# Kernel tuning notes

Hardware: AMD Instinct MI355X
Metric: run time of the kernel (lower is better)

Reference implementation:

```python
import jax, jax.numpy as jnp
import numpy as np
from jax.scipy.special import xlogy

LAMBDA_XM = 0.05
LAMBDA_SEG2D = 1.0
BN_EPS = 1e-5


def setup_inputs() -> dict:
    key = jax.random.key(0)
    ks = jax.random.split(key, 40)
    S, N, Nv, B, Np, M, H, C, MID = 2, 240000, 80000, 2, 120000, 30000, 64, 20, 16
    Nimg = B * M
    f = lambda i, shape, s=0.05: jax.random.normal(ks[i], shape, jnp.float32) * s
    inp = {
        'img_feat': f(0, (S, Nimg, H), 1.0),
        'pts_feat': f(1, (S, Nv, H), 1.0),
        'coors_inv': jax.random.randint(ks[2], (S, N), 0, Nv),
        'labels': jax.random.randint(ks[3], (N,), 0, C),
        'img_label': jax.random.randint(ks[4], (Nimg,), 0, C),
        'p2img_idx': jax.random.randint(ks[5], (B, M), 0, Np),
        # multihead 3d classifiers (per scale): Linear(H,128)-ReLU-Linear(128,C)
        'w3a': f(6, (S, H, 128)), 'b3a': jnp.zeros((S, 128)),
        'w3b': f(7, (S, 128, C)), 'b3b': jnp.zeros((S, C)),
        # multihead fuse classifiers
        'wfa': f(8, (S, H, 128)), 'bfa': jnp.zeros((S, 128)),
        'wfb': f(9, (S, 128, C)), 'bfb': jnp.zeros((S, C)),
        # attention: fc1(H->H//4), fc2(H->H//4), fc3(H//2->2), conv1/conv2 (1x1 -> linear) + BN
        'fc1w': f(10, (S, H, MID)), 'fc1b': jnp.zeros((S, MID)),
        'fc2w': f(11, (S, H, MID)), 'fc2b': jnp.zeros((S, MID)),
        'fc3w': f(12, (S, 2 * MID, 2)), 'fc3b': jnp.zeros((S, 2)),
        'c1w': f(13, (S, H, H)), 'c1b': jnp.zeros((S, H)),
        'bn1g': jnp.ones((S, H)), 'bn1b': jnp.zeros((S, H)),
        'c2w': f(14, (S, H, H)), 'c2b': jnp.zeros((S, H)),
        'bn2g': jnp.ones((S, H)), 'bn2b': jnp.zeros((S, H)),
        # final classifier Linear(S*H,128)-ReLU-Linear(128,C)
        'clw1': f(15, (S * H, 128)), 'clb1': jnp.zeros((128,)),
        'clw2': f(16, (128, C)), 'clb2': jnp.zeros((C,)),
    }
    return inp


def _mlp2(x, w1, b1, w2, b2):
    return jax.nn.relu(x @ w1 + b1) @ w2 + b2


def _ce(logits, lab):
    logp = jax.nn.log_softmax(logits, -1)
    return -jnp.take_along_axis(logp, lab[:, None], axis=1).mean()


def _lovasz(probs, lab):
    # lovasz-softmax over all classes, averaged over present classes
    C = probs.shape[1]
    fg = jax.nn.one_hot(lab, C, dtype=probs.dtype)  # [N,C]
    errors = jnp.abs(fg - probs)

    def per_class(err_c, fg_c):
        order = jnp.argsort(-err_c)
        e = err_c[order]
        f = fg_c[order]
        gts = f.sum()
        inter = gts - jnp.cumsum(f)
        union = gts + jnp.cumsum(1.0 - f)
        jac = 1.0 - inter / union
        jac = jnp.concatenate([jac[:1], jac[1:] - jac[:-1]])
        return jnp.dot(e, jac)

    losses = jax.vmap(per_class)(errors.T, fg.T)  # [C]
    present = (fg.sum(0) > 0).astype(probs.dtype)
    return jnp.sum(losses * present) / jnp.maximum(present.sum(), 1.0)


def _seg_loss(logits, lab):
    return _ce(logits, lab) + _lovasz(jax.nn.softmax(logits, -1), lab)


def _convbn_relu(x, cw, cb, g, b):
    # 1x1 Conv1d == per-point linear; BN (training-mode batch stats over points)
    y = x @ cw + cb
    mu = y.mean(0)
    var = y.var(0)
    return jax.nn.relu((y - mu) * jax.lax.rsqrt(var + BN_EPS) * g + b)


def reference(img_feat, pts_feat, coors_inv, labels, img_label, p2img_idx,
              w3a, b3a, w3b, b3b, wfa, bfa, wfb, bfb,
              fc1w, fc1b, fc2w, fc2b, fc3w, fc3b,
              c1w, c1b, bn1g, bn1b, c2w, c2b, bn2g, bn2b,
              clw1, clb1, clw2, clb2):
    S, Nv, H = pts_feat.shape
    C = w3b.shape[-1]
    B, M = p2img_idx.shape
    N = labels.shape[0]
    Np = N // B
    # p2img_mapping: per-batch gather composed to one global gather (batch blocks are contiguous/equal)
    gidx = (jnp.arange(B)[:, None] * Np + p2img_idx).reshape(-1)  # [Nimg]

    loss = jnp.float32(0.0)
    feats = []
    for s in range(S):
        pred3d = _mlp2(pts_feat[s], w3a[s], b3a[s], w3b[s], b3b[s])  # [Nv,C]
        # voxelize_labels: majority vote per voxel (== unique+scatter_max count argmax)
        counts = jnp.zeros((Nv, C), jnp.float32).at[coors_inv[s], labels].add(1.0)
        vox_lab = jnp.argmax(counts, axis=1)  # [Nv]
        # gather voxel feats/preds to image-projected points (fused gather)
        idx = coors_inv[s][gidx]  # [Nimg]
        p = pts_feat[s][idx]      # [Nimg,H] pseudo feats
        pts_pred = pred3d[idx]    # [Nimg,C]
        v = img_feat[s]           # [Nimg,H] valid (image) feats
        # Attention fusion
        w = jax.nn.sigmoid(
            jnp.concatenate([p @ fc1w[s] + fc1b[s], v @ fc2w[s] + fc2b[s]], -1) @ fc3w[s] + fc3b[s])  # [Nimg,2]
        fuse = (_convbn_relu(p, c1w[s], c1b[s], bn1g[s], bn1b[s]) * w[:, 0:1]
                + _convbn_relu(v, c2w[s], c2b[s], bn2g[s], bn2b[s]) * w[:, 1:2])
        feats.append(fuse)
        fuse_pred = _mlp2(fuse, wfa[s], bfa[s], wfb[s], bfb[s])
        loss = loss + _seg_loss(pred3d, vox_lab)
        loss = loss + _seg_loss(fuse_pred, img_label) * LAMBDA_SEG2D / S
        # F.kl_div(log_softmax(pts_pred), softmax(fuse_pred)), reduction='mean' over all elements
        pf = jax.nn.softmax(fuse_pred, -1)
        kl = jnp.mean(xlogy(pf, pf) - pf * jax.nn.log_softmax(pts_pred, -1))
        loss = loss + kl * LAMBDA_XM / S
    img_logits = _mlp2(jnp.concatenate(feats, -1), clw1, clb1, clw2, clb2)
    loss = loss + _seg_loss(img_logits, img_label)
    return loss
```

## Files before the change

kernel.cpp:

```cpp
#include <hip/hip_runtime.h>
#include <stdint.h>

static constexpr int NV   = 80000;
static constexpr int NPT  = 240000;
static constexpr int NIMG = 60000;
static constexpr int Hh   = 64;
static constexpr int Cc   = 20;
static constexpr int NPp  = 120000;
static constexpr int Mm   = 30000;
static constexpr int NB     = 8192;
static constexpr int NCH    = 16;
static constexpr int NBLK_GA  = (NIMG + 63) / 64;
static constexpr int NBLK_MLP = NV / 64;
static constexpr int NBLK_CNT = (NPT + 255) / 256;
static constexpr int NBLK_FILL_NV = (NV + 255) / 256;
static constexpr int NBLK_FILL_NI = (NIMG + 255) / 256;
static constexpr int NBLK_HIST = Cc * NCH;
static constexpr int NBLK_IDX  = (NIMG + 255) / 256;
#define BN_EPS 1e-5f

using bf16x8 = __attribute__((ext_vector_type(8))) short;
using f32x4  = __attribute__((ext_vector_type(4))) float;

__device__ __forceinline__ float waveReduce(float v) {
  #pragma unroll
  for (int o = 32; o > 0; o >>= 1) v += __shfl_down(v, o);
  return v;
}
__device__ __forceinline__ short f2bf(float f) {
  uint32_t u = __float_as_uint(f);
  return (short)((u + 0x7FFFu + ((u >> 16) & 1u)) >> 16);
}
__device__ __forceinline__ float bf2f(uint32_t h) { return __uint_as_float(h << 16); }
__device__ __forceinline__ uint32_t pk2(float a, float b) {
  return ((uint32_t)(uint16_t)f2bf(a)) | ((uint32_t)(uint16_t)f2bf(b) << 16);
}

struct PackDesc { const float* src; short* dst; int K, Nr, nt; };
struct PackArgs { PackDesc d[14]; };

__global__ void __launch_bounds__(256)
k_pack_zero(PackArgs pa,
            const float* __restrict__ fc1w, const float* __restrict__ fc1b,
            const float* __restrict__ fc2w, const float* __restrict__ fc2b,
            const float* __restrict__ fc3w, const float* __restrict__ fc3b,
            float* __restrict__ attEffs,
            uint4* __restrict__ zb, int zq,
            const int* __restrict__ ci0, const int* __restrict__ ci1,
            const int* __restrict__ p2img,
            int* __restrict__ idx0, int* __restrict__ idx1) {
  int bid = blockIdx.x;
  if (bid >= 384) {
    bid -= 384;
    if (bid < NBLK_IDX) {
      int i = bid * 256 + threadIdx.x;
      if (i < NIMG) idx0[i] = ci0[(i >= Mm ? NPp : 0) + p2img[i]];
    } else {
      int i = (bid - NBLK_IDX) * 256 + threadIdx.x;
      if (i < NIMG) idx1[i] = ci1[(i >= Mm ? NPp : 0) + p2img[i]];
    }
    return;
  }
  if (bid >= 128) {
    const uint4 z = make_uint4(0u, 0u, 0u, 0u);
    int i = (bid - 128) * 256 + threadIdx.x;
    for (; i < zq; i += 256 * 256) zb[i] = z;
    return;
  }
  const int stride = 128 * 256;
  for (int di = 0; di < 14; di++) {
    const float* src = pa.d[di].src;
    short* dst = pa.d[di].dst;
    int K = pa.d[di].K, Nr = pa.d[di].Nr, ntiles = pa.d[di].nt;
    int total = (K / 32) * ntiles * 512;
    for (int idx = bid * 256 + threadIdx.x; idx < total; idx += stride) {
      int j = idx & 7, lane = (idx >> 3) & 63, tile = idx >> 9;
      int nt = tile % ntiles, kt = tile / ntiles;
      int k = kt * 32 + (lane >> 4) * 8 + j;
      int n = nt * 16 + (lane & 15);
      float v = (n < Nr) ? src[(size_t)k * Nr + n] : 0.f;
      dst[idx] = f2bf(v);
    }
  }
  if (bid < 2 && threadIdx.x < 64) {
    int s = bid, t = threadIdx.x;
    const float* f1w = fc1w + s * 64 * 16; const float* f1b = fc1b + s * 16;
    const float* f2w = fc2w + s * 64 * 16; const float* f2b = fc2b + s * 16;
    const float* f3w = fc3w + s * 64;      const float* f3b = fc3b + s * 2;
    float* aE = attEffs + s * 320;
    float p0 = 0.f, p1 = 0.f, v0 = 0.f, v1 = 0.f;
    #pragma unroll
    for (int j = 0; j < 16; j++) {
      p0 = fmaf(f1w[t * 16 + j], f3w[j * 2], p0);
      p1 = fmaf(f1w[t * 16 + j], f3w[j * 2 + 1], p1);
      v0 = fmaf(f2w[t * 16 + j], f3w[(16 + j) * 2], v0);
      v1 = fmaf(f2w[t * 16 + j], f3w[(16 + j) * 2 + 1], v1);
    }
    aE[t * 2] = p0; aE[t * 2 + 1] = p1;
    aE[128 + t * 2] = v0; aE[128 + t * 2 + 1] = v1;
    if (t == 0) {
      float b0 = f3b[0], b1 = f3b[1];
      for (int j = 0; j < 16; j++) {
        b0 += f1b[j] * f3w[j * 2] + f2b[j] * f3w[(16 + j) * 2];
        b1 += f1b[j] * f3w[j * 2 + 1] + f2b[j] * f3w[(16 + j) * 2 + 1];
      }
      aE[256] = b0; aE[257] = b1;
    }
  }
}

__device__ void scanbin_body(const uint32_t* __restrict__ Hb, const uint32_t* __restrict__ HFb,
                             int n, int call, float* __restrict__ lossesC5,
                             int* __restrict__ gts5, int cls) {
  __shared__ int sWC[4], sWF[4];
  __shared__ float sRedF[4];
  int t = threadIdx.x;
  int lane = t & 63, w = t >> 6;
  const uint32_t* Hc  = Hb  + (size_t)cls * NB;
  const uint32_t* HFc = HFb + (size_t)cls * NB;
  int locC = 0, locF = 0;
  #pragma unroll
  for (int i = 0; i < 8; i++) {
    uint4 cv = *(const uint4*)(Hc  + t * 32 + i * 4);
    uint4 fv = *(const uint4*)(HFc + t * 32 + i * 4);
    locC += (int)(cv.x + cv.y + cv.z + cv.w);
    locF += (int)(fv.x + fv.y + fv.z + fv.w);
  }
  int sc = locC, sf = locF;
  #pragma unroll
  for (int o = 1; o < 64; o <<= 1) {
    int a = __shfl_up(sc, o);
    int b = __shfl_up(sf, o);
    if (lane >= o) { sc += a; sf += b; }
  }
  if (lane == 63) { sWC[w] = sc; sWF[w] = sf; }
  __syncthreads();
  int offC = 0, offF = 0, Ftot = 0;
  #pragma unroll
  for (int ww = 0; ww < 4; ww++) {
    int fc = sWF[ww];
    Ftot += fc;
    if (ww < w) { offC += sWC[ww]; offF += fc; }
  }
  int runC = offC + sc - locC;
  int runF = offF + sf - locF;
  float gts = (float)Ftot;
  float contrib = 0.f;
  #pragma unroll
  for (int i = 0; i < 8; i++) {
    uint4 cv = *(const uint4*)(Hc  + t * 32 + i * 4);
    uint4 fv = *(const uint4*)(HFc + t * 32 + i * 4);
    uint32_t ca[4] = {cv.x, cv.y, cv.z, cv.w};
    uint32_t fa[4] = {fv.x, fv.y, fv.z, fv.w};
    #pragma unroll
    for (int j = 0; j < 4; j++) {
      int cnt = (int)ca[j], fgc = (int)fa[j];
      runC += cnt; runF += fgc;
      if (cnt > 0 && Ftot > 0) {
        float r0 = (float)(n - runC);
        float F0 = (float)(Ftot - runF);
        float r1 = r0 + (float)cnt;
        float F1 = F0 + (float)fgc;
        float emean = __uint_as_float((uint32_t)(t * 32 + i * 4 + j) << 17);
        contrib += emean * (r1 / (gts + r1 - F1) - r0 / (gts + r0 - F0));
      }
    }
  }
  contrib = waveReduce(contrib);
  if (lane == 0) sRedF[w] = contrib;
  __syncthreads();
  if (t == 0) {
    lossesC5[call * 32 + cls] = (Ftot > 0) ? (sRedF[0] + sRedF[1] + sRedF[2] + sRedF[3]) : 0.f;
    gts5[call * 32 + cls] = Ftot;
  }
}

template<int D>
__device__ __forceinline__ void mfma_mlp_body(const short* sXb, short* sH,
    int r0, int rows,
    const short* __restrict__ pw1, const float* __restrict__ B1,
    const short* __restrict__ pw2, const float* __restrict__ B2,
    float* __restrict__ Out) {
  constexpr int LDB = D + 8;
  constexpr int KT1 = D / 32;
  const int t = threadIdx.x;
  const int lane = t & 63, w = t >> 6;
  const int m = lane & 15, quad = lane >> 4;
  const int rowA = 16 * w + m;
  bf16x8 a1[KT1];
  #pragma unroll
  for (int kt = 0; kt < KT1; kt++)
    a1[kt] = *(const bf16x8*)(sXb + rowA * LDB + kt * 32 + quad * 8);
  const bf16x8* b1 = (const bf16x8*)pw1;
  #pragma unroll
  for (int nt = 0; nt < 8; nt++) {
    f32x4 c = {0.f, 0.f, 0.f, 0.f};
    #pragma unroll
    for (int kt = 0; kt < KT1; kt++)
      c = __builtin_amdgcn_mfma_f32_16x16x32_bf16(a1[kt], b1[(kt * 8 + nt) * 64 + lane], c, 0, 0, 0);
    int col = nt * 16 + m;
    float bc = B1[col];
    #pragma unroll
    for (int reg = 0; reg < 4; reg++)
      sH[(16 * w + quad * 4 + reg) * 136 + col] = f2bf(fmaxf(c[reg] + bc, 0.f));
  }
  __syncthreads();
  bf16x8 a2[4];
  #pragma unroll
  for (int kt = 0; kt < 4; kt++)
    a2[kt] = *(const bf16x8*)(sH + rowA * 136 + kt * 32 + quad * 8);
  const bf16x8* b2 = (const bf16x8*)pw2;
  #pragma unroll
  for (int nt = 0; nt < 2; nt++) {
    f32x4 c = {0.f, 0.f, 0.f, 0.f};
    #pragma unroll
    for (int kt = 0; kt < 4; kt++)
      c = __builtin_amdgcn_mfma_f32_16x16x32_bf16(a2[kt], b2[(kt * 2 + nt) * 64 + lane], c, 0, 0, 0);
    int col = nt * 16 + m;
    if (col < Cc) {
      float bc = B2[col];
      #pragma unroll
      for (int reg = 0; reg < 4; reg++) {
        int gr = r0 + 16 * w + quad * 4 + reg;
        if (gr < rows) Out[(size_t)gr * Cc + col] = c[reg] + bc;
      }
    }
  }
}

__device__ void mlp64_body(int bid0, const float* __restrict__ X,
    const short* __restrict__ pw1, const float* __restrict__ B1,
    const short* __restrict__ pw2, const float* __restrict__ B2,
    float* __restrict__ Out, int rows, char* smem) {
  short* sXb = (short*)smem;
  short* sH  = (short*)(smem + 9216);
  int t = threadIdx.x, r0 = bid0 * 64;
  for (int i = t; i < 1024; i += 256) {
    int r = i >> 4, k4 = (i & 15) * 4;
    int gr = r0 + r;
    float4 v = (gr < rows) ? *(const float4*)(X + (size_t)gr * 64 + k4)
                           : make_float4(0.f, 0.f, 0.f, 0.f);
    uint2 p; p.x = pk2(v.x, v.y); p.y = pk2(v.z, v.w);
    *(uint2*)(sXb + r * 72 + k4) = p;
  }
  __syncthreads();
  mfma_mlp_body<64>(sXb, sH, r0, rows, pw1, B1, pw2, B2, Out);
}

__device__ void mlp128_body(int bid0, const uint16_t* __restrict__ Xh,
    const short* __restrict__ pw1, const float* __restrict__ B1,
    const short* __restrict__ pw2, const float* __restrict__ B2,
    float* __restrict__ Out, char* smem) {
  short* sXb = (short*)smem;
  short* sH  = (short*)(smem + 17408);
  int t = threadIdx.x, r0 = bid0 * 64;
  for (int i = t; i < 2048; i += 256) {
    int r = i >> 5, k4 = (i & 31) * 4;
    int gr = r0 + r;
    uint2 p = (gr < NIMG) ? *(const uint2*)(Xh + (size_t)gr * 128 + k4) : make_uint2(0u, 0u);
    *(uint2*)(sXb + r * 136 + k4) = p;
  }
  __syncthreads();
  mfma_mlp_body<128>(sXb, sH, r0, NIMG, pw1, B1, pw2, B2, Out);
}

__device__ void cnt_body(int bid0, const int* __restrict__ ci, const int* __restrict__ labels,
                         int* __restrict__ counts) {
  int i = bid0 * 256 + threadIdx.x;
  if (i < NPT) atomicAdd(&counts[(size_t)ci[i] * Cc + labels[i]], 1);
}

__device__ void colred_body(int bid0, const float* __restrict__ partials,
                            float* __restrict__ red64) {
  int t = threadIdx.x, j = bid0;
  float v = 0.f;
  for (int b = j; b < NBLK_GA; b += 64) v += partials[(size_t)b * 256 + t];
  red64[j * 256 + t] = v;
}

__device__ void fill_body(int bid0, const float* __restrict__ logits,
                          const int* __restrict__ lab, const int* __restrict__ vcnt,
                          int n, uint16_t* __restrict__ E,
                          float ceScale, float* __restrict__ lossAcc,
                          const float* __restrict__ pred3d, const int* __restrict__ idxg,
                          float klScale) {
  int i = bid0 * 256 + threadIdx.x;
  float total = 0.f;
  if (i < n) {
    int lb;
    if (vcnt) {
      const int* crow = vcnt + (size_t)i * Cc;
      int best = crow[0], arg = 0;
      #pragma unroll
      for (int k = 1; k < Cc; k++) {
        int ck = crow[k];
        if (ck > best) { best = ck; arg = k; }
      }
      lb = arg;
    } else {
      lb = lab[i];
    }
    const float* l = logits + (size_t)i * Cc;
    float m = l[0];
    #pragma unroll
    for (int c = 1; c < Cc; c++) m = fmaxf(m, l[c]);
    float ex[Cc]; float se = 0.f;
    #pragma unroll
    for (int c = 0; c < Cc; c++) { ex[c] = expf(l[c] - m); se += ex[c]; }
    float inv = 1.f / se;
    float lse = logf(se);
    total = -(l[lb] - m - lse) * ceScale;
    #pragma unroll
    for (int c = 0; c < Cc; c++) {
      float prob = ex[c] * inv;
      int fg = (c == lb) ? 1 : 0;
      float err = fg ? (1.f - prob) : prob;
      err = fmaxf(err, 0.f);
      uint32_t key = __float_as_uint(err) >> 17;
      E[(size_t)c * n + i] = (uint16_t)((key << 1) | (uint32_t)fg);
    }
    if (pred3d) {
      const float* q = pred3d + (size_t)idxg[i] * Cc;
      float mq = q[0];
      #pragma unroll
      for (int c = 1; c < Cc; c++) mq = fmaxf(mq, q[c]);
      float sq = 0.f;
      #pragma unroll
      for (int c = 0; c < Cc; c++) sq += expf(q[c] - mq);
      float lsq = logf(sq);
      float kl = 0.f;
      #pragma unroll
      for (int c = 0; c < Cc; c++) {
        float lf = l[c] - m - lse;
        float pf = ex[c] * inv;
        float lq = q[c] - mq - lsq;
        kl += pf * (lf - lq);
      }
      total += kl * klScale;
    }
  }
  total = waveReduce(total);
  __shared__ float sh[4];
  int lane = threadIdx.x & 63, w = threadIdx.x >> 6;
  if (lane == 0) sh[w] = total;
  __syncthreads();
  if (threadIdx.x == 0) atomicAdd(lossAcc, sh[0] + sh[1] + sh[2] + sh[3]);
}

__device__ void hist_body(int bid0, const uint16_t* __restrict__ E, int n,
                          uint32_t* __restrict__ H, uint32_t* __restrict__ HF, char* smem) {
  uint32_t* lcf = (uint32_t*)smem;
  int t = threadIdx.x;
  int cls = bid0 / NCH, ch = bid0 - cls * NCH;
  int CHsz = (n + NCH - 1) / NCH;
  int i0 = ch * CHsz;
  int i1 = min(n, i0 + CHsz);
  for (int b = t; b < NB; b += 256) lcf[b] = 0u;
  __syncthreads();
  const uint16_t* Ec = E + (size_t)cls * n;
  for (int i = i0 + t; i < i1; i += 256) {
    uint32_t p = Ec[i];
    atomicAdd(&lcf[p >> 1], 0x10000u | (p & 1u));
  }
  __syncthreads();
  uint32_t* Hc  = H  + (size_t)cls * NB;
  uint32_t* HFc = HF + (size_t)cls * NB;
  for (int b = t; b < NB; b += 256) {
    uint32_t v = lcf[b];
    if (v) {
      atomicAdd(&Hc[b], v >> 16);
      uint32_t f = v & 0xFFFFu;
      if (f) atomicAdd(&HFc[b], f);
    }
  }
}

__device__ void gatt_body(int bid0, const float* __restrict__ pts, const int* __restrict__ idx,
                          const float* __restrict__ img,
                          const short* __restrict__ pc1, const float* __restrict__ c1b,
                          const short* __restrict__ pc2, const float* __restrict__ c2b,
                          const float* __restrict__ attEff,
                          uint16_t* __restrict__ y1, uint16_t* __restrict__ y2,
                          float* __restrict__ attw, float* __restrict__ partials,
                          char* smem) {
  short* sP = (short*)smem;
  short* sV = (short*)(smem + 9216);
  float* sAtt  = (float*)(smem + 18432);
  float* sStat = (float*)(smem + 20480);
  int t = threadIdx.x;
  int r0 = bid0 * 64;
  for (int i = t; i < 1024; i += 256) {
    int r = i >> 4, q = i & 15;
    int gr = r0 + r;
    float4 vp = make_float4(0.f, 0.f, 0.f, 0.f), vv = vp;
    if (gr < NIMG) {
      vp = *(const float4*)(pts + (size_t)idx[gr] * 64 + q * 4);
      vv = *(const float4*)(img + (size_t)gr * 64 + q * 4);
    }
    uint2 pp, qv;
    pp.x = pk2(vp.x, vp.y); pp.y = pk2(vp.z, vp.w);
    qv.x = pk2(vv.x, vv.y); qv.y = pk2(vv.z, vv.w);
    *(uint2*)(sP + r * 72 + q * 4) = pp;
    *(uint2*)(sV + r * 72 + q * 4) = qv;
  }
  __syncthreads();
  {
    int r = t & 63, qq = t >> 6;
    const float* aP = attEff;
    const float* aV = attEff + 128;
    float l0 = 0.f, l1 = 0.f;
    for (int k = qq * 16; k < qq * 16 + 16; k += 4) {
      uint2 up = *(const uint2*)(sP + r * 72 + k);
      uint2 uv = *(const uint2*)(sV + r * 72 + k);
      float p0 = bf2f(up.x & 0xffff), p1 = bf2f(up.x >> 16);
      float p2 = bf2f(up.y & 0xffff), p3 = bf2f(up.y >> 16);
      float v0 = bf2f(uv.x & 0xffff), v1 = bf2f(uv.x >> 16);
      float v2 = bf2f(uv.y & 0xffff), v3 = bf2f(uv.y >> 16);
      float4 wa = *(const float4*)(aP + 2 * k);
      float4 wb = *(const float4*)(aP + 2 * k + 4);
      l0 += p0 * wa.x + p1 * wa.z + p2 * wb.x + p3 * wb.z;
      l1 += p0 * wa.y + p1 * wa.w + p2 * wb.y + p3 * wb.w;
      float4 ua = *(const float4*)(aV + 2 * k);
      float4 ub = *(const float4*)(aV + 2 * k + 4);
      l0 += v0 * ua.x + v1 * ua.z + v2 * ub.x + v3 * ub.z;
      l1 += v0 * ua.y + v1 * ua.w + v2 * ub.y + v3 * ub.w;
    }
    sAtt[r * 8 + qq * 2] = l0;
    sAtt[r * 8 + qq * 2 + 1] = l1;
  }
  const int lane = t & 63, w = t >> 6;
  const int m = lane & 15, quad = lane >> 4;
  const int rowA = 16 * w + m;
  bf16x8 ap[2], av[2];
  #pragma unroll
  for (int kt = 0; kt < 2; kt++) {
    ap[kt] = *(const bf16x8*)(sP + rowA * 72 + kt * 32 + quad * 8);
    av[kt] = *(const bf16x8*)(sV + rowA * 72 + kt * 32 + quad * 8);
  }
  const bf16x8* b1 = (const bf16x8*)pc1;
  const bf16x8* b2 = (const bf16x8*)pc2;
  #pragma unroll
  for (int nt = 0; nt < 4; nt++) {
    int col = nt * 16 + m;
    f32x4 c1 = {0.f, 0.f, 0.f, 0.f}, c2 = {0.f, 0.f, 0.f, 0.f};
    #pragma unroll
    for (int kt = 0; kt < 2; kt++) {
      c1 = __builtin_amdgcn_mfma_f32_16x16x32_bf16(ap[kt], b1[(kt * 4 + nt) * 64 + lane], c1, 0, 0, 0);
      c2 = __builtin_amdgcn_mfma_f32_16x16x32_bf16(av[kt], b2[(kt * 4 + nt) * 64 + lane], c2, 0, 0, 0);
    }
    float bb1 = c1b[col], bb2 = c2b[col];
    float s1 = 0.f, q1 = 0.f, s2 = 0.f, q2 = 0.f;
    #pragma unroll
    for (int reg = 0; reg < 4; reg++) {
      int gr = r0 + 16 * w + quad * 4 + reg;
      if (gr < NIMG) {
// ... 48 lines not shown
    float* __restrict__ Out, char* smem) {
  short* sXb = (short*)smem;
  short* sH  = (short*)(smem + 9216);
  float* sBn = (float*)(smem + 9216 + 17408);
  int t = threadIdx.x, r0 = bid0 * 64;
  float acc = 0.f;
  #pragma unroll 8
  for (int b = 0; b < 64; b++) acc += red64[b * 256 + t];
  float* sSum = (float*)sH;
  sSum[t] = acc;
  __syncthreads();
  if (t < 64) {
    float nn = (float)NIMG;
    float mu1 = sSum[t] / nn;
    float var1 = sSum[64 + t] / nn - mu1 * mu1;
    float a1 = g1[t] / sqrtf(var1 + BN_EPS);
    sBn[t] = a1; sBn[64 + t] = be1[t] - mu1 * a1;
    float mu2 = sSum[128 + t] / nn;
    float var2 = sSum[192 + t] / nn - mu2 * mu2;
    float a2 = g2[t] / sqrtf(var2 + BN_EPS);
    sBn[128 + t] = a2; sBn[192 + t] = be2[t] - mu2 * a2;
  }
  __syncthreads();
  for (int i = t; i < 1024; i += 256) {
    int r = i >> 4, q = i & 15;
    int gr = r0 + r;
    uint2 zp = make_uint2(0u, 0u);
    if (gr < NIMG) {
      float4 a1 = *(const float4*)(sBn + q * 4);
      float4 c1 = *(const float4*)(sBn + 64 + q * 4);
      float4 a2 = *(const float4*)(sBn + 128 + q * 4);
      float4 c2 = *(const float4*)(sBn + 192 + q * 4);
      uint2 u1 = *(const uint2*)(y1 + (size_t)gr * 64 + q * 4);
      uint2 u2 = *(const uint2*)(y2 + (size_t)gr * 64 + q * 4);
      float w0 = attw[gr * 2], w1 = attw[gr * 2 + 1];
      float zx = fmaxf(fmaf(bf2f(u1.x & 0xffff), a1.x, c1.x), 0.f) * w0
               + fmaxf(fmaf(bf2f(u2.x & 0xffff), a2.x, c2.x), 0.f) * w1;
      float zy = fmaxf(fmaf(bf2f(u1.x >> 16),   a1.y, c1.y), 0.f) * w0
               + fmaxf(fmaf(bf2f(u2.x >> 16),   a2.y, c2.y), 0.f) * w1;
      float zz = fmaxf(fmaf(bf2f(u1.y & 0xffff), a1.z, c1.z), 0.f) * w0
               + fmaxf(fmaf(bf2f(u2.y & 0xffff), a2.z, c2.z), 0.f) * w1;
      float zw = fmaxf(fmaf(bf2f(u1.y >> 16),   a1.w, c1.w), 0.f) * w0
               + fmaxf(fmaf(bf2f(u2.y >> 16),   a2.w, c2.w), 0.f) * w1;
      zp.x = pk2(zx, zy); zp.y = pk2(zz, zw);
      *(uint2*)(feats + (size_t)gr * 128 + s64 + q * 4) = zp;
    }
    *(uint2*)(sXb + r * 72 + q * 4) = zp;
  }
  __syncthreads();
  mfma_mlp_body<64>(sXb, sH, r0, NIMG, pw1, B1, pw2, B2, Out);
}

__global__ void __launch_bounds__(256)
k_mega2(const float* __restrict__ pf0, const float* __restrict__ pf1,
        const int* __restrict__ idx0, const int* __restrict__ idx1,
        const float* __restrict__ if0, const float* __restrict__ if1,
        const short* pc1w0, const short* pc1w1, const short* pc2w0, const short* pc2w1,
        const float* c1b, const float* c2b, const float* attEffs,
        uint16_t* y1a, uint16_t* y2a, uint16_t* y1b, uint16_t* y2b,
        float* attw0, float* attw1, float* partials0, float* partials1,
        const short* pw3a0, const float* b3a, const short* pw3b0, const float* b3b,
        const short* pw3a1, const short* pw3b1,
        float* pred3d0, float* pred3d1,
        const int* __restrict__ ci0, const int* __restrict__ ci1,
        const int* __restrict__ labels,
        int* __restrict__ counts0, int* __restrict__ counts1) {
  __shared__ char smem[26624];
  int bid = blockIdx.x;
  if (bid < NBLK_GA) {
    gatt_body(bid, pf0, idx0, if0, pc1w0, c1b, pc2w0, c2b, attEffs,
              y1a, y2a, attw0, partials0, smem);
    return;
  }
  bid -= NBLK_GA;
  if (bid < NBLK_GA) {
    gatt_body(bid, pf1, idx1, if1, pc1w1, c1b + 64, pc2w1, c2b + 64, attEffs + 320,
              y1b, y2b, attw1, partials1, smem);
    return;
  }
  bid -= NBLK_GA;
  if (bid < NBLK_MLP) { mlp64_body(bid, pf0, pw3a0, b3a, pw3b0, b3b, pred3d0, NV, smem); return; }
  bid -= NBLK_MLP;
  if (bid < NBLK_MLP) { mlp64_body(bid, pf1, pw3a1, b3a + 128, pw3b1, b3b + Cc, pred3d1, NV, smem); return; }
  bid -= NBLK_MLP;
  if (bid < NBLK_CNT) { cnt_body(bid, ci0, labels, counts0); return; }
  cnt_body(bid - NBLK_CNT, ci1, labels, counts1);
}

__global__ void __launch_bounds__(256)
k_fill_colred(const float* __restrict__ l0, const int* __restrict__ vc0, uint16_t* __restrict__ E0,
              const float* __restrict__ l1, const int* __restrict__ vc1, uint16_t* __restrict__ E1,
              float ce, float* __restrict__ lossAcc,
              const float* partials0, float* red64_0,
              const float* partials1, float* red64_1) {
  int bid = blockIdx.x;
  if (bid < NBLK_FILL_NV) {
    fill_body(bid, l0, nullptr, vc0, NV, E0, ce, lossAcc, nullptr, nullptr, 0.f);
    return;
  }
  bid -= NBLK_FILL_NV;
  if (bid < NBLK_FILL_NV) {
    fill_body(bid, l1, nullptr, vc1, NV, E1, ce, lossAcc, nullptr, nullptr, 0.f);
    return;
  }
  bid -= NBLK_FILL_NV;
  if (bid < 64) { colred_body(bid, partials0, red64_0); return; }
  colred_body(bid - 64, partials1, red64_1);
}

__global__ void __launch_bounds__(256)
k_fuse2_hist2(const uint16_t* y1a, const uint16_t* y2a, const float* attw0, const float* red64_0,
              const uint16_t* y1b, const uint16_t* y2b, const float* attw1, const float* red64_1,
              const float* bn1g, const float* bn1b, const float* bn2g, const float* bn2b,
              uint16_t* feats,
              const short* pwfa0, const float* bfa, const short* pwfb0, const float* bfb,
              const short* pwfa1, const short* pwfb1,
              float* fusepred0, float* fusepred1,
              const uint16_t* __restrict__ E0, uint32_t* H0, uint32_t* HF0,
              const uint16_t* __restrict__ E1, uint32_t* H2, uint32_t* HF2) {
  __shared__ char smem[32768];
  int bid = blockIdx.x;
  if (bid < NBLK_GA) {
    fusemlp_body(bid, y1a, y2a, attw0, red64_0, bn1g, bn1b, bn2g, bn2b, feats, 0,
                 pwfa0, bfa, pwfb0, bfb, fusepred0, smem);
    return;
  }
  bid -= NBLK_GA;
  if (bid < NBLK_GA) {
    fusemlp_body(bid, y1b, y2b, attw1, red64_1, bn1g + 64, bn1b + 64, bn2g + 64, bn2b + 64,
                 feats, 64, pwfa1, bfa + 128, pwfb1, bfb + Cc, fusepred1, smem);
    return;
  }
  bid -= NBLK_GA;
  if (bid < NBLK_HIST) { hist_body(bid, E0, NV, H0, HF0, smem); return; }
  hist_body(bid - NBLK_HIST, E1, NV, H2, HF2, smem);
}

__global__ void __launch_bounds__(256)
k_finx2(const uint16_t* __restrict__ feats,
        const short* pcl1, const float* clb1, const short* pcl2, const float* clb2,
        float* finalpred,
        const float* fusepred0, const float* pred3d0, const int* idx0, uint16_t* E0w,
        const float* fusepred1, const float* pred3d1, const int* idx1, uint16_t* E1w,
        const int* __restrict__ img_label, float ce, float kl, float* lossAcc,
        const uint32_t* H0, const uint32_t* HF0,
        const uint32_t* H2, const uint32_t* HF2,
        float* lossesC5, int* gts5) {
  __shared__ char smem[34816];
  int bid = blockIdx.x;
  if (bid < NBLK_GA) { mlp128_body(bid, feats, pcl1, clb1, pcl2, clb2, finalpred, smem); return; }
  bid -= NBLK_GA;
  if (bid < NBLK_FILL_NI) {
    fill_body(bid, fusepred0, img_label, nullptr, NIMG, E0w, ce, lossAcc, pred3d0, idx0, kl);
    return;
  }
  bid -= NBLK_FILL_NI;
  if (bid < NBLK_FILL_NI) {
    fill_body(bid, fusepred1, img_label, nullptr, NIMG, E1w, ce, lossAcc, pred3d1, idx1, kl);
    return;
  }
  bid -= NBLK_FILL_NI;
  if (bid < Cc) { scanbin_body(H0, HF0, NV, 0, lossesC5, gts5, bid); return; }
  scanbin_body(H2, HF2, NV, 2, lossesC5, gts5, bid - Cc);
}

__global__ void __launch_bounds__(256)
k_hist2_fill(const uint16_t* __restrict__ E0, uint32_t* H1, uint32_t* HF1,
             const uint16_t* __restrict__ E1, uint32_t* H3, uint32_t* HF3,
             const float* __restrict__ finalpred, const int* __restrict__ img_label,
             uint16_t* __restrict__ E2, float ce, float* lossAcc) {
  __shared__ char smem[32768];
  int bid = blockIdx.x;
  if (bid < NBLK_HIST) { hist_body(bid, E0, NIMG, H1, HF1, smem); return; }
  bid -= NBLK_HIST;
  if (bid < NBLK_HIST) { hist_body(bid, E1, NIMG, H3, HF3, smem); return; }
  fill_body(bid - NBLK_HIST, finalpred, img_label, nullptr, NIMG, E2, ce, lossAcc,
            nullptr, nullptr, 0.f);
}

__global__ void __launch_bounds__(256)
k_hist_scan2(const uint16_t* __restrict__ E2, uint32_t* H4, uint32_t* HF4,
             const uint32_t* H1, const uint32_t* HF1,
             const uint32_t* H3, const uint32_t* HF3,
             float* lossesC5, int* gts5) {
  __shared__ char smem[32768];
  int bid = blockIdx.x;
  if (bid < NBLK_HIST) { hist_body(bid, E2, NIMG, H4, HF4, smem); return; }
  bid -= NBLK_HIST;
  if (bid < Cc) { scanbin_body(H1, HF1, NIMG, 1, lossesC5, gts5, bid); return; }
  scanbin_body(H3, HF3, NIMG, 3, lossesC5, gts5, bid - Cc);
}

__global__ void __launch_bounds__(256)
k_scanbin5(const uint32_t* Hb, const uint32_t* HFb, int n, int call,
           float* lossesC5, int* gts5) {
  scanbin_body(Hb, HFb, n, call, lossesC5, gts5, blockIdx.x);
}

__global__ void k_final(const float* __restrict__ lossAcc,
                        const float* __restrict__ lossesC5, const int* __restrict__ gts5,
                        float* __restrict__ out) {
  const float coefs[5] = {1.0f, 0.5f, 1.0f, 0.5f, 1.0f};
  float loss = lossAcc[0];
  for (int call = 0; call < 5; call++) {
    float s = 0.f; int np = 0;
    for (int c = 0; c < Cc; c++)
      if (gts5[call * 32 + c] > 0) { s += lossesC5[call * 32 + c]; np++; }
    loss += coefs[call] * s / (float)(np > 0 ? np : 1);
  }
  out[0] = loss;
}

extern "C" void kernel_launch(void* const* d_in, const int* in_sizes, int n_in,
                              void* d_out, int out_size, void* d_ws, size_t ws_size,
                              hipStream_t stream) {
  const float* img_feat = (const float*)d_in[0];
  const float* pts_feat = (const float*)d_in[1];
  const int* coors_inv  = (const int*)d_in[2];
  const int* labels     = (const int*)d_in[3];
  const int* img_label  = (const int*)d_in[4];
  const int* p2img      = (const int*)d_in[5];
  const float* w3a = (const float*)d_in[6];
  const float* b3a = (const float*)d_in[7];
  const float* w3b = (const float*)d_in[8];
  const float* b3b = (const float*)d_in[9];
  const float* wfa = (const float*)d_in[10];
  const float* bfa = (const float*)d_in[11];
  const float* wfb = (const float*)d_in[12];
  const float* bfb = (const float*)d_in[13];
  const float* fc1w = (const float*)d_in[14];
  const float* fc1b = (const float*)d_in[15];
  const float* fc2w = (const float*)d_in[16];
  const float* fc2b = (const float*)d_in[17];
  const float* fc3w = (const float*)d_in[18];
  const float* fc3b = (const float*)d_in[19];
  const float* c1w  = (const float*)d_in[20];
  const float* c1b  = (const float*)d_in[21];
  const float* bn1g = (const float*)d_in[22];
  const float* bn1b = (const float*)d_in[23];
  const float* c2w  = (const float*)d_in[24];
  const float* c2b  = (const float*)d_in[25];
  const float* bn2g = (const float*)d_in[26];
  const float* bn2b = (const float*)d_in[27];
  const float* clw1 = (const float*)d_in[28];
  const float* clb1 = (const float*)d_in[29];
  const float* clw2 = (const float*)d_in[30];
  const float* clb2 = (const float*)d_in[31];
  (void)in_sizes; (void)n_in; (void)out_size; (void)ws_size;

  char* ws = (char*)d_ws;
  size_t off = 0;
  auto alloc = [&](size_t bytes) { void* p = ws + off; off += (bytes + 255) & ~(size_t)255; return p; };
  uint16_t* feats = (uint16_t*)alloc((size_t)NIMG * 128 * 2);
  float* pred3d0 = (float*)alloc((size_t)NV * Cc * 4);
  float* pred3d1 = (float*)alloc((size_t)NV * Cc * 4);
  int* idx0 = (int*)alloc((size_t)NIMG * 4);
  int* idx1 = (int*)alloc((size_t)NIMG * 4);
  uint16_t* y1a = (uint16_t*)alloc((size_t)NIMG * Hh * 2);
  uint16_t* y2a = (uint16_t*)alloc((size_t)NIMG * Hh * 2);
  uint16_t* y1b = (uint16_t*)alloc((size_t)NIMG * Hh * 2);
  uint16_t* y2b = (uint16_t*)alloc((size_t)NIMG * Hh * 2);
  uint16_t* E0 = (uint16_t*)alloc((size_t)Cc * NV * 2);
  uint16_t* E1 = (uint16_t*)alloc((size_t)Cc * NV * 2);
  uint16_t* E2 = (uint16_t*)alloc((size_t)Cc * NIMG * 2);
  float* partials0 = (float*)alloc((size_t)NBLK_GA * 256 * 4);
  float* partials1 = (float*)alloc((size_t)NBLK_GA * 256 * 4);
  float* red64_0 = (float*)alloc(64 * 256 * 4);
  float* red64_1 = (float*)alloc(64 * 256 * 4);
  float* attw0 = (float*)alloc((size_t)NIMG * 2 * 4);
  float* attw1 = (float*)alloc((size_t)NIMG * 2 * 4);
  float* fusepred0 = (float*)alloc((size_t)NIMG * Cc * 4);
  float* fusepred1 = (float*)alloc((size_t)NIMG * Cc * 4);
  float* finalpred = (float*)alloc((size_t)NIMG * Cc * 4);
  short* pwAll = (short*)alloc(86016 * 2);
  short* pw3a0 = pwAll,          * pw3a1 = pwAll + 8192;
  short* pwfa0 = pwAll + 16384,  * pwfa1 = pwAll + 24576;
  short* pw3b0 = pwAll + 32768,  * pw3b1 = pwAll + 36864;
  short* pwfb0 = pwAll + 40960,  * pwfb1 = pwAll + 45056;
  short* pcl1  = pwAll + 49152;
  short* pcl2  = pwAll + 65536;
  short* pc1w0 = pwAll + 69632,  * pc1w1 = pwAll + 73728;
  short* pc2w0 = pwAll + 77824,  * pc2w1 = pwAll + 81920;
  float* attEffs = (float*)alloc(2 * 320 * 4);
  size_t zsize = 1024 + (size_t)5 * 2 * Cc * NB * 4 + (size_t)2 * NV * Cc * 4;
  char* zbase = (char*)alloc(zsize);
  float* lossAcc  = (float*)zbase;
  float* lossesC5 = (float*)zbase + 32;
  int*   gts5     = (int*)((float*)zbase + 192);
  uint32_t* Hbase = (uint32_t*)(zbase + 1024);
  auto Hc  = [&](int call) { return Hbase + (size_t)call * 2 * Cc * NB; };
  auto HFc = [&](int call) { return Hbase + (size_t)call * 2 * Cc * NB + (size_t)Cc * NB; };
  int* counts0 = (int*)(zbase + 1024 + (size_t)5 * 2 * Cc * NB * 4);
  int* counts1 = counts0 + (size_t)NV * Cc;
  int zq = (int)(zsize / 16);

  const float kl = 0.025f / ((float)NIMG * Cc);
  const float* pf0 = pts_feat;
  const float* pf1 = pts_feat + (size_t)NV * Hh;
  const float* if0 = img_feat;
  const float* if1 = img_feat + (size_t)NIMG * Hh;
  const int* ci0 = coors_inv;
  const int* ci1 = coors_inv + NPT;

  PackArgs pa;
  pa.d[0]  = {w3a,        pw3a0, 64, 128, 8};
  pa.d[1]  = {w3a + 8192, pw3a1, 64, 128, 8};
  pa.d[2]  = {wfa,        pwfa0, 64, 128, 8};
  pa.d[3]  = {wfa + 8192, pwfa1, 64, 128, 8};
  pa.d[4]  = {w3b,        pw3b0, 128, 20, 2};
  pa.d[5]  = {w3b + 2560, pw3b1, 128, 20, 2};
  pa.d[6]  = {wfb,        pwfb0, 128, 20, 2};
  pa.d[7]  = {wfb + 2560, pwfb1, 128, 20, 2};
  pa.d[8]  = {clw1,       pcl1, 128, 128, 8};
  pa.d[9]  = {clw2,       pcl2, 128, 20, 2};
  pa.d[10] = {c1w,        pc1w0, 64, 64, 4};
  pa.d[11] = {c1w + 4096, pc1w1, 64, 64, 4};
  pa.d[12] = {c2w,        pc2w0, 64, 64, 4};
  pa.d[13] = {c2w + 4096, pc2w1, 64, 64, 4};
  k_pack_zero<<<384 + 2 * NBLK_IDX, 256, 0, stream>>>(
      pa, fc1w, fc1b, fc2w, fc2b, fc3w, fc3b, attEffs,
      (uint4*)zbase, zq, ci0, ci1, p2img, idx0, idx1);

  k_mega2<<<2 * NBLK_GA + 2 * NBLK_MLP + 2 * NBLK_CNT, 256, 0, stream>>>(
      pf0, pf1, idx0, idx1, if0, if1,
      pc1w0, pc1w1, pc2w0, pc2w1, c1b, c2b, attEffs,
      y1a, y2a, y1b, y2b, attw0, attw1, partials0, partials1,
      pw3a0, b3a, pw3b0, b3b, pw3a1, pw3b1, pred3d0, pred3d1,
      ci0, ci1, labels, counts0, counts1);

  k_fill_colred<<<2 * NBLK_FILL_NV + 128, 256, 0, stream>>>(
      pred3d0, counts0, E0, pred3d1, counts1, E1, 1.0f / NV, lossAcc,
      partials0, red64_0, partials1, red64_1);

  k_fuse2_hist2<<<2 * NBLK_GA + 2 * NBLK_HIST, 256, 0, stream>>>(
      y1a, y2a, attw0, red64_0, y1b, y2b, attw1, red64_1,
      bn1g, bn1b, bn2g, bn2b, feats,
      pwfa0, bfa, pwfb0, bfb, pwfa1, pwfb1, fusepred0, fusepred1,
      E0, Hc(0), HFc(0), E1, Hc(2), HFc(2));

  k_finx2<<<NBLK_GA + 2 * NBLK_FILL_NI + 2 * Cc, 256, 0, stream>>>(
      feats, pcl1, clb1, pcl2, clb2, finalpred,
      fusepred0, pred3d0, idx0, E0,
      fusepred1, pred3d1, idx1, E1,
      img_label, 0.5f / NIMG, kl, lossAcc,
      Hc(0), HFc(0), Hc(2), HFc(2), lossesC5, gts5);

  k_hist2_fill<<<2 * NBLK_HIST + NBLK_FILL_NI, 256, 0, stream>>>(
      E0, Hc(1), HFc(1), E1, Hc(3), HFc(3),
      finalpred, img_label, E2, 1.0f / NIMG, lossAcc);

  k_hist_scan2<<<NBLK_HIST + 2 * Cc, 256, 0, stream>>>(
      E2, Hc(4), HFc(4), Hc(1), HFc(1), Hc(3), HFc(3), lossesC5, gts5);

  k_scanbin5<<<Cc, 256, 0, stream>>>(Hc(4), HFc(4), NIMG, 4, lossesC5, gts5);

  k_final<<<1, 1, 0, stream>>>(lossAcc, lossesC5, gts5, (float*)d_out);
}
```

Baseline: 347.1 us.

## Pre-convert point features to bf16, pack histograms into 64-bit bins, interleave blocks

```diff
diff --git a/kernel.cpp b/kernel.cpp
--- a/kernel.cpp
+++ b/kernel.cpp
@@ -17,6 +17,7 @@
 static constexpr int NBLK_FILL_NI = (NIMG + 255) / 256;
 static constexpr int NBLK_HIST = Cc * NCH;
 static constexpr int NBLK_IDX  = (NIMG + 255) / 256;
+static constexpr int NBLK_CVT  = 1280;
 #define BN_EPS 1e-5f
 
 using bf16x8 = __attribute__((ext_vector_type(8))) short;
@@ -48,8 +49,24 @@
             uint4* __restrict__ zb, int zq,
             const int* __restrict__ ci0, const int* __restrict__ ci1,
             const int* __restrict__ p2img,
-            int* __restrict__ idx0, int* __restrict__ idx1) {
+            int* __restrict__ idx0, int* __restrict__ idx1,
+            const float* __restrict__ pts, uint16_t* __restrict__ ptsbf) {
   int bid = blockIdx.x;
+  if (bid >= 384 + 2 * NBLK_IDX) {
+    int i = (bid - 384 - 2 * NBLK_IDX) * 256 + threadIdx.x;
+    const int total8 = 2 * NV * 64 / 8;
+    const int strideC = NBLK_CVT * 256;
+    for (; i < total8; i += strideC) {
+      const float* s = pts + (size_t)i * 8;
+      float4 a = *(const float4*)s;
+      float4 b = *(const float4*)(s + 4);
+      uint4 o;
+      o.x = pk2(a.x, a.y); o.y = pk2(a.z, a.w);
+      o.z = pk2(b.x, b.y); o.w = pk2(b.z, b.w);
+      *(uint4*)(ptsbf + (size_t)i * 8) = o;
+    }
+    return;
+  }
   if (bid >= 384) {
     bid -= 384;
     if (bid < NBLK_IDX) {
@@ -109,22 +126,20 @@
   }
 }
 
-__device__ void scanbin_body(const uint32_t* __restrict__ Hb, const uint32_t* __restrict__ HFb,
+__device__ void scanbin_body(const unsigned long long* __restrict__ H64,
                              int n, int call, float* __restrict__ lossesC5,
                              int* __restrict__ gts5, int cls) {
   __shared__ int sWC[4], sWF[4];
   __shared__ float sRedF[4];
   int t = threadIdx.x;
   int lane = t & 63, w = t >> 6;
-  const uint32_t* Hc  = Hb  + (size_t)cls * NB;
-  const uint32_t* HFc = HFb + (size_t)cls * NB;
+  const uint4* Hv = (const uint4*)(H64 + (size_t)cls * NB + (size_t)t * 32);
   int locC = 0, locF = 0;
   #pragma unroll
-  for (int i = 0; i < 8; i++) {
-    uint4 cv = *(const uint4*)(Hc  + t * 32 + i * 4);
-    uint4 fv = *(const uint4*)(HFc + t * 32 + i * 4);
-    locC += (int)(cv.x + cv.y + cv.z + cv.w);
-    locF += (int)(fv.x + fv.y + fv.z + fv.w);
+  for (int i = 0; i < 16; i++) {
+    uint4 u = Hv[i];
+    locF += (int)(u.x + u.z);
+    locC += (int)(u.y + u.w);
   }
   int sc = locC, sf = locF;
   #pragma unroll
@@ -147,21 +162,18 @@
   float gts = (float)Ftot;
   float contrib = 0.f;
   #pragma unroll
-  for (int i = 0; i < 8; i++) {
-    uint4 cv = *(const uint4*)(Hc  + t * 32 + i * 4);
-    uint4 fv = *(const uint4*)(HFc + t * 32 + i * 4);
-    uint32_t ca[4] = {cv.x, cv.y, cv.z, cv.w};
-    uint32_t fa[4] = {fv.x, fv.y, fv.z, fv.w};
-    #pragma unroll
-    for (int j = 0; j < 4; j++) {
-      int cnt = (int)ca[j], fgc = (int)fa[j];
+  for (int i = 0; i < 16; i++) {
+    uint4 u = Hv[i];
+    #pragma unroll
+    for (int j = 0; j < 2; j++) {
+      int cnt = (int)(j ? u.w : u.y), fgc = (int)(j ? u.z : u.x);
       runC += cnt; runF += fgc;
       if (cnt > 0 && Ftot > 0) {
         float r0 = (float)(n - runC);
         float F0 = (float)(Ftot - runF);
         float r1 = r0 + (float)cnt;
         float F1 = F0 + (float)fgc;
-        float emean = __uint_as_float((uint32_t)(t * 32 + i * 4 + j) << 17);
+        float emean = __uint_as_float((uint32_t)(t * 32 + i * 2 + j) << 17);
         contrib += emean * (r1 / (gts + r1 - F1) - r0 / (gts + r0 - F0));
       }
     }
@@ -228,20 +240,19 @@
   }
 }
 
-__device__ void mlp64_body(int bid0, const float* __restrict__ X,
+__device__ void mlp64bf_body(int bid0, const uint16_t* __restrict__ Xh,
     const short* __restrict__ pw1, const float* __restrict__ B1,
     const short* __restrict__ pw2, const float* __restrict__ B2,
     float* __restrict__ Out, int rows, char* smem) {
   short* sXb = (short*)smem;
   short* sH  = (short*)(smem + 9216);
   int t = threadIdx.x, r0 = bid0 * 64;
-  for (int i = t; i < 1024; i += 256) {
-    int r = i >> 4, k4 = (i & 15) * 4;
+  for (int i = t; i < 512; i += 256) {
+    int r = i >> 3, k8 = (i & 7) * 8;
     int gr = r0 + r;
-    float4 v = (gr < rows) ? *(const float4*)(X + (size_t)gr * 64 + k4)
-                           : make_float4(0.f, 0.f, 0.f, 0.f);
-    uint2 p; p.x = pk2(v.x, v.y); p.y = pk2(v.z, v.w);
-    *(uint2*)(sXb + r * 72 + k4) = p;
+    uint4 p = (gr < rows) ? *(const uint4*)(Xh + (size_t)gr * 64 + k8)
+                          : make_uint4(0u, 0u, 0u, 0u);
+    *(uint4*)(sXb + r * 72 + k8) = p;
   }
   __syncthreads();
   mfma_mlp_body<64>(sXb, sH, r0, rows, pw1, B1, pw2, B2, Out);
@@ -348,7 +359,7 @@
 }
 
 __device__ void hist_body(int bid0, const uint16_t* __restrict__ E, int n,
-                          uint32_t* __restrict__ H, uint32_t* __restrict__ HF, char* smem) {
+                          unsigned long long* __restrict__ H64, char* smem) {
   uint32_t* lcf = (uint32_t*)smem;
   int t = threadIdx.x;
   int cls = bid0 / NCH, ch = bid0 - cls * NCH;
@@ -363,19 +374,16 @@
     atomicAdd(&lcf[p >> 1], 0x10000u | (p & 1u));
   }
   __syncthreads();
-  uint32_t* Hc  = H  + (size_t)cls * NB;
-  uint32_t* HFc = HF + (size_t)cls * NB;
+  unsigned long long* Hc = H64 + (size_t)cls * NB;
   for (int b = t; b < NB; b += 256) {
     uint32_t v = lcf[b];
-    if (v) {
-      atomicAdd(&Hc[b], v >> 16);
-      uint32_t f = v & 0xFFFFu;
-      if (f) atomicAdd(&HFc[b], f);
-    }
-  }
-}
-
-__device__ void gatt_body(int bid0, const float* __restrict__ pts, const int* __restrict__ idx,
+    if (v)
+      atomicAdd(&Hc[b], ((unsigned long long)(v >> 16) << 32) | (v & 0xFFFFu));
+  }
+}
+
+__device__ void gatt_body(int bid0, const uint16_t* __restrict__ ptsbf,
+                          const int* __restrict__ idx,
                           const float* __restrict__ img,
                           const short* __restrict__ pc1, const float* __restrict__ c1b,
                           const short* __restrict__ pc2, const float* __restrict__ c2b,
@@ -389,18 +397,20 @@
   float* sStat = (float*)(smem + 20480);
   int t = threadIdx.x;
   int r0 = bid0 * 64;
+  for (int i = t; i < 512; i += 256) {
+    int r = i >> 3, q = i & 7;
+    int gr = r0 + r;
+    uint4 pv = make_uint4(0u, 0u, 0u, 0u);
+    if (gr < NIMG) pv = *(const uint4*)(ptsbf + (size_t)idx[gr] * 64 + q * 8);
+    *(uint4*)(sP + r * 72 + q * 8) = pv;
+  }
   for (int i = t; i < 1024; i += 256) {
     int r = i >> 4, q = i & 15;
     int gr = r0 + r;
-    float4 vp = make_float4(0.f, 0.f, 0.f, 0.f), vv = vp;
-    if (gr < NIMG) {
-      vp = *(const float4*)(pts + (size_t)idx[gr] * 64 + q * 4);
-      vv = *(const float4*)(img + (size_t)gr * 64 + q * 4);
-    }
-    uint2 pp, qv;
-    pp.x = pk2(vp.x, vp.y); pp.y = pk2(vp.z, vp.w);
+    float4 vv = make_float4(0.f, 0.f, 0.f, 0.f);
+    if (gr < NIMG) vv = *(const float4*)(img + (size_t)gr * 64 + q * 4);
+    uint2 qv;
     qv.x = pk2(vv.x, vv.y); qv.y = pk2(vv.z, vv.w);
-    *(uint2*)(sP + r * 72 + q * 4) = pp;
     *(uint2*)(sV + r * 72 + q * 4) = qv;
   }
   __syncthreads();
@@ -555,7 +565,7 @@
 }
 
 __global__ void __launch_bounds__(256)
-k_mega2(const float* __restrict__ pf0, const float* __restrict__ pf1,
+k_mega2(const uint16_t* __restrict__ pb0, const uint16_t* __restrict__ pb1,
         const int* __restrict__ idx0, const int* __restrict__ idx1,
         const float* __restrict__ if0, const float* __restrict__ if1,
         const short* pc1w0, const short* pc1w1, const short* pc2w0, const short* pc2w1,
@@ -570,24 +580,31 @@
         int* __restrict__ counts0, int* __restrict__ counts1) {
   __shared__ char smem[26624];
   int bid = blockIdx.x;
-  if (bid < NBLK_GA) {
-    gatt_body(bid, pf0, idx0, if0, pc1w0, c1b, pc2w0, c2b, attEffs,
-              y1a, y2a, attw0, partials0, smem);
-    return;
-  }
-  bid -= NBLK_GA;
-  if (bid < NBLK_GA) {
-    gatt_body(bid, pf1, idx1, if1, pc1w1, c1b + 64, pc2w1, c2b + 64, attEffs + 320,
-              y1b, y2b, attw1, partials1, smem);
-    return;
-  }
-  bid -= NBLK_GA;
-  if (bid < NBLK_MLP) { mlp64_body(bid, pf0, pw3a0, b3a, pw3b0, b3b, pred3d0, NV, smem); return; }
-  bid -= NBLK_MLP;
-  if (bid < NBLK_MLP) { mlp64_body(bid, pf1, pw3a1, b3a + 128, pw3b1, b3b + Cc, pred3d1, NV, smem); return; }
-  bid -= NBLK_MLP;
-  if (bid < NBLK_CNT) { cnt_body(bid, ci0, labels, counts0); return; }
-  cnt_body(bid - NBLK_CNT, ci1, labels, counts1);
+  if (bid < 2 * NBLK_CNT) {
+    if (bid < NBLK_CNT) cnt_body(bid, ci0, labels, counts0);
+    else cnt_body(bid - NBLK_CNT, ci1, labels, counts1);
+    return;
+  }
+  bid -= 2 * NBLK_CNT;
+  if (bid < 4 * NBLK_GA) {
+    int h = bid >> 1;
+    if (bid & 1) {
+      if (h < NBLK_MLP)
+        mlp64bf_body(h, pb0, pw3a0, b3a, pw3b0, b3b, pred3d0, NV, smem);
+      else
+        mlp64bf_body(h - NBLK_MLP, pb1, pw3a1, b3a + 128, pw3b1, b3b + Cc, pred3d1, NV, smem);
+    } else {
+      if (h < NBLK_GA)
+        gatt_body(h, pb0, idx0, if0, pc1w0, c1b, pc2w0, c2b, attEffs,
+                  y1a, y2a, attw0, partials0, smem);
+      else
+        gatt_body(h - NBLK_GA, pb1, idx1, if1, pc1w1, c1b + 64, pc2w1, c2b + 64,
+                  attEffs + 320, y1b, y2b, attw1, partials1, smem);
+    }
+    return;
+  }
+  bid -= 4 * NBLK_GA;
+  mlp64bf_body(626 + bid, pb1, pw3a1, b3a + 128, pw3b1, b3b + Cc, pred3d1, NV, smem);
 }
 
 __global__ void __launch_bounds__(256)
@@ -619,8 +636,8 @@
               const short* pwfa0, const float* bfa, const short* pwfb0, const float* bfb,
               const short* pwfa1, const short* pwfb1,
               float* fusepred0, float* fusepred1,
-              const uint16_t* __restrict__ E0, uint32_t* H0, uint32_t* HF0,
-              const uint16_t* __restrict__ E1, uint32_t* H2, uint32_t* HF2) {
+              const uint16_t* __restrict__ E0, unsigned long long* H0,
+              const uint16_t* __restrict__ E1, unsigned long long* H2) {
   __shared__ char smem[32768];
   int bid = blockIdx.x;
   if (bid < NBLK_GA) {
@@ -635,8 +652,8 @@
     return;
   }
   bid -= NBLK_GA;
-  if (bid < NBLK_HIST) { hist_body(bid, E0, NV, H0, HF0, smem); return; }
-  hist_body(bid - NBLK_HIST, E1, NV, H2, HF2, smem);
+  if (bid < NBLK_HIST) { hist_body(bid, E0, NV, H0, smem); return; }
+  hist_body(bid - NBLK_HIST, E1, NV, H2, smem);
 }
 
 __global__ void __launch_bounds__(256)
@@ -646,8 +663,7 @@
         const float* fusepred0, const float* pred3d0, const int* idx0, uint16_t* E0w,
         const float* fusepred1, const float* pred3d1, const int* idx1, uint16_t* E1w,
         const int* __restrict__ img_label, float ce, float kl, float* lossAcc,
-        const uint32_t* H0, const uint32_t* HF0,
-        const uint32_t* H2, const uint32_t* HF2,
+        const unsigned long long* H0, const unsigned long long* H2,
         float* lossesC5, int* gts5) {
   __shared__ char smem[34816];
   int bid = blockIdx.x;
@@ -663,41 +679,40 @@
     return;
   }
   bid -= NBLK_FILL_NI;
-  if (bid < Cc) { scanbin_body(H0, HF0, NV, 0, lossesC5, gts5, bid); return; }
-  scanbin_body(H2, HF2, NV, 2, lossesC5, gts5, bid - Cc);
+  if (bid < Cc) { scanbin_body(H0, NV, 0, lossesC5, gts5, bid); return; }
+  scanbin_body(H2, NV, 2, lossesC5, gts5, bid - Cc);
 }
 
 __global__ void __launch_bounds__(256)
-k_hist2_fill(const uint16_t* __restrict__ E0, uint32_t* H1, uint32_t* HF1,
-             const uint16_t* __restrict__ E1, uint32_t* H3, uint32_t* HF3,
+k_hist2_fill(const uint16_t* __restrict__ E0, unsigned long long* H1,
+             const uint16_t* __restrict__ E1, unsigned long long* H3,
              const float* __restrict__ finalpred, const int* __restrict__ img_label,
              uint16_t* __restrict__ E2, float ce, float* lossAcc) {
   __shared__ char smem[32768];
   int bid = blockIdx.x;
-  if (bid < NBLK_HIST) { hist_body(bid, E0, NIMG, H1, HF1, smem); return; }
+  if (bid < NBLK_HIST) { hist_body(bid, E0, NIMG, H1, smem); return; }
   bid -= NBLK_HIST;
-  if (bid < NBLK_HIST) { hist_body(bid, E1, NIMG, H3, HF3, smem); return; }
+  if (bid < NBLK_HIST) { hist_body(bid, E1, NIMG, H3, smem); return; }
   fill_body(bid - NBLK_HIST, finalpred, img_label, nullptr, NIMG, E2, ce, lossAcc,
             nullptr, nullptr, 0.f);
 }
 
 __global__ void __launch_bounds__(256)
-k_hist_scan2(const uint16_t* __restrict__ E2, uint32_t* H4, uint32_t* HF4,
-             const uint32_t* H1, const uint32_t* HF1,
-             const uint32_t* H3, const uint32_t* HF3,
+k_hist_scan2(const uint16_t* __restrict__ E2, unsigned long long* H4,
+             const unsigned long long* H1, const unsigned long long* H3,
              float* lossesC5, int* gts5) {
   __shared__ char smem[32768];
   int bid = blockIdx.x;
-  if (bid < NBLK_HIST) { hist_body(bid, E2, NIMG, H4, HF4, smem); return; }
+  if (bid < NBLK_HIST) { hist_body(bid, E2, NIMG, H4, smem); return; }
   bid -= NBLK_HIST;
-  if (bid < Cc) { scanbin_body(H1, HF1, NIMG, 1, lossesC5, gts5, bid); return; }
-  scanbin_body(H3, HF3, NIMG, 3, lossesC5, gts5, bid - Cc);
+  if (bid < Cc) { scanbin_body(H1, NIMG, 1, lossesC5, gts5, bid); return; }
+  scanbin_body(H3, NIMG, 3, lossesC5, gts5, bid - Cc);
 }
 
 __global__ void __launch_bounds__(256)
-k_scanbin5(const uint32_t* Hb, const uint32_t* HFb, int n, int call,
+k_scanbin5(const unsigned long long* H64, int n, int call,
            float* lossesC5, int* gts5) {
-  scanbin_body(Hb, HFb, n, call, lossesC5, gts5, blockIdx.x);
+  scanbin_body(H64, n, call, lossesC5, gts5, blockIdx.x);
 }
 
 __global__ void k_final(const float* __restrict__ lossAcc,
@@ -755,6 +770,7 @@
   size_t off = 0;
   auto alloc = [&](size_t bytes) { void* p = ws + off; off += (bytes + 255) & ~(size_t)255; return p; };
   uint16_t* feats = (uint16_t*)alloc((size_t)NIMG * 128 * 2);
+  uint16_t* ptsbf = (uint16_t*)alloc((size_t)2 * NV * Hh * 2);
   float* pred3d0 = (float*)alloc((size_t)NV * Cc * 4);
   float* pred3d1 = (float*)alloc((size_t)NV * Cc * 4);
   int* idx0 = (int*)alloc((size_t)NIMG * 4);
@@ -785,25 +801,24 @@
   short* pc1w0 = pwAll + 69632,  * pc1w1 = pwAll + 73728;
   short* pc2w0 = pwAll + 77824,  * pc2w1 = pwAll + 81920;
   float* attEffs = (float*)alloc(2 * 320 * 4);
-  size_t zsize = 1024 + (size_t)5 * 2 * Cc * NB * 4 + (size_t)2 * NV * Cc * 4;
+  size_t zsize = 1024 + (size_t)5 * Cc * NB * 8 + (size_t)2 * NV * Cc * 4;
   char* zbase = (char*)alloc(zsize);
   float* lossAcc  = (float*)zbase;
   float* lossesC5 = (float*)zbase + 32;
   int*   gts5     = (int*)((float*)zbase + 192);
-  uint32_t* Hbase = (uint32_t*)(zbase + 1024);
-  auto Hc  = [&](int call) { return Hbase + (size_t)call * 2 * Cc * NB; };
-  auto HFc = [&](int call) { return Hbase + (size_t)call * 2 * Cc * NB + (size_t)Cc * NB; };
-  int* counts0 = (int*)(zbase + 1024 + (size_t)5 * 2 * Cc * NB * 4);
+  unsigned long long* Hbase = (unsigned long long*)(zbase + 1024);
+  auto Hc = [&](int call) { return Hbase + (size_t)call * Cc * NB; };
+  int* counts0 = (int*)(zbase + 1024 + (size_t)5 * Cc * NB * 8);
   int* counts1 = counts0 + (size_t)NV * Cc;
   int zq = (int)(zsize / 16);
 
   const float kl = 0.025f / ((float)NIMG * Cc);
-  const float* pf0 = pts_feat;
-  const float* pf1 = pts_feat + (size_t)NV * Hh;
   const float* if0 = img_feat;
   const float* if1 = img_feat + (size_t)NIMG * Hh;
   const int* ci0 = coors_inv;
   const int* ci1 = coors_inv + NPT;
+  uint16_t* pb0 = ptsbf;
+  uint16_t* pb1 = ptsbf + (size_t)NV * Hh;
 
   PackArgs pa;
   pa.d[0]  = {w3a,        pw3a0, 64, 128, 8};
@@ -820,12 +835,12 @@
   pa.d[11] = {c1w + 4096, pc1w1, 64, 64, 4};
   pa.d[12] = {c2w,        pc2w0, 64, 64, 4};
   pa.d[13] = {c2w + 4096, pc2w1, 64, 64, 4};
-  k_pack_zero<<<384 + 2 * NBLK_IDX, 256, 0, stream>>>(
+  k_pack_zero<<<384 + 2 * NBLK_IDX + NBLK_CVT, 256, 0, stream>>>(
       pa, fc1w, fc1b, fc2w, fc2b, fc3w, fc3b, attEffs,
-      (uint4*)zbase, zq, ci0, ci1, p2img, idx0, idx1);
-
-  k_mega2<<<2 * NBLK_GA + 2 * NBLK_MLP + 2 * NBLK_CNT, 256, 0, stream>>>(
-      pf0, pf1, idx0, idx1, if0, if1,
+      (uint4*)zbase, zq, ci0, ci1, p2img, idx0, idx1, pts_feat, ptsbf);
+
+  k_mega2<<<2 * NBLK_CNT + 4 * NBLK_GA + 2 * (NBLK_MLP - NBLK_GA), 256, 0, stream>>>(
+      pb0, pb1, idx0, idx1, if0, if1,
       pc1w0, pc1w1, pc2w0, pc2w1, c1b, c2b, attEffs,
       y1a, y2a, y1b, y2b, attw0, attw1, partials0, partials1,
       pw3a0, b3a, pw3b0, b3b, pw3a1, pw3b1, pred3d0, pred3d1,
@@ -839,23 +854,23 @@
       y1a, y2a, attw0, red64_0, y1b, y2b, attw1, red64_1,
       bn1g, bn1b, bn2g, bn2b, feats,
       pwfa0, bfa, pwfb0, bfb, pwfa1, pwfb1, fusepred0, fusepred1,
-      E0, Hc(0), HFc(0), E1, Hc(2), HFc(2));
+      E0, Hc(0), E1, Hc(2));
 
   k_finx2<<<NBLK_GA + 2 * NBLK_FILL_NI + 2 * Cc, 256, 0, stream>>>(
       feats, pcl1, clb1, pcl2, clb2, finalpred,
       fusepred0, pred3d0, idx0, E0,
       fusepred1, pred3d1, idx1, E1,
       img_label, 0.5f / NIMG, kl, lossAcc,
-      Hc(0), HFc(0), Hc(2), HFc(2), lossesC5, gts5);
+      Hc(0), Hc(2), lossesC5, gts5);
 
   k_hist2_fill<<<2 * NBLK_HIST + NBLK_FILL_NI, 256, 0, stream>>>(
-      E0, Hc(1), HFc(1), E1, Hc(3), HFc(3),
+      E0, Hc(1), E1, Hc(3),
       finalpred, img_label, E2, 1.0f / NIMG, lossAcc);
 
   k_hist_scan2<<<NBLK_HIST + 2 * Cc, 256, 0, stream>>>(
-      E2, Hc(4), HFc(4), Hc(1), HFc(1), Hc(3), HFc(3), lossesC5, gts5);
-
-  k_scanbin5<<<Cc, 256, 0, stream>>>(Hc(4), HFc(4), NIMG, 4, lossesC5, gts5);
+      E2, Hc(4), Hc(1), Hc(3), lossesC5, gts5);
+
+  k_scanbin5<<<Cc, 256, 0, stream>>>(Hc(4), NIMG, 4, lossesC5, gts5);
 
   k_final<<<1, 1, 0, stream>>>(lossAcc, lossesC5, gts5, (float*)d_out);
 }
```

Result: slower. 362.9 us (+4.6%).
